# Performance work log

Measured on AMD Instinct MI355X. Metric: run time of the kernel, lower is better.

The kernel has to match this reference:

```python
import jax, jax.numpy as jnp
import numpy as np

K = 16       # patchsize
STRIDE = 4
C1 = 1e-6
C2 = 1e-6


def _unfold(x):
    # Mirrors nn.Unfold(kernel_size=16, stride=4) followed by
    # .view(a,b,k,k,-1).transpose(2,4): output (a,b,pt_num,k,k) where the
    # trailing (k,k) matrix is the TRANSPOSED patch (kw,kh), exactly as in torch.
    a, b, H, W = x.shape
    nh = (H - K) // STRIDE + 1
    nw = (W - K) // STRIDE + 1
    r = (jnp.arange(nh) * STRIDE)[:, None] + jnp.arange(K)[None, :]  # (nh,K)
    c = (jnp.arange(nw) * STRIDE)[:, None] + jnp.arange(K)[None, :]  # (nw,K)
    p = x[:, :, r[:, None, :, None], c[None, :, None, :]]  # (a,b,nh,nw,K,K) = (kh,kw)
    p = p.reshape(a, b, nh * nw, K, K)
    return jnp.swapaxes(p, -1, -2)  # transposed patch, matching transpose(2,4)


def _layer(ref_f, dist_f):
    # ref_f, dist_f: (a,b,H,W) feature maps of one VGG layer
    pr = _unfold(ref_f)   # (a,b,pt,K,K)
    pd = _unfold(dist_f)
    u_r, s_r, _ = jnp.linalg.svd(pr, full_matrices=False)  # u:(a,b,pt,K,K) s:(a,b,pt,K)
    u_d, s_d, _ = jnp.linalg.svd(pd, full_matrices=False)
    diff_s = (s_r - s_d) ** 2                               # (a,b,pt,K)
    # abs of elementwise U product summed over singular-vector index (sign-invariant)
    u_rd = jnp.abs(u_r * u_d).sum(-1)                       # (a,b,pt,K)
    wt = jnp.std(u_rd, axis=-1, ddof=1) / (jnp.mean(u_rd, axis=-1) + 1e-9)  # (a,b,pt)
    ds = (diff_s.sum(-1) * wt).mean(-1).mean(-1)            # (a,)
    # global luminance-similarity weighting
    xm = dist_f.mean(axis=(2, 3))                           # (a,b)
    ym = ref_f.mean(axis=(2, 3))
    s1 = (2.0 * xm * ym + C1) / (xm ** 2 + ym ** 2 + C2)
    glb = jnp.exp(-2.0 * s1.mean(axis=1))                   # (a,)
    return ds * glb


def setup_inputs() -> dict:
    key = jax.random.key(0)
    k1, k2, k3, k4 = jax.random.split(key, 4)
    return {
        "ref_feat3": jax.random.normal(k1, (4, 256, 64, 64), jnp.float32),
        "dist_feat3": jax.random.normal(k2, (4, 256, 64, 64), jnp.float32),
        "ref_feat4": jax.random.normal(k3, (4, 512, 32, 32), jnp.float32),
        "dist_feat4": jax.random.normal(k4, (4, 512, 32, 32), jnp.float32),
    }


def reference(ref_feat3, dist_feat3, ref_feat4, dist_feat4):
    # DMM accumulates the weighted singular-value distance over the two feature levels
    return _layer(ref_feat3, dist_feat3) + _layer(ref_feat4, dist_feat4)
```

## Files before the change

kernel.cpp:

```cpp
#include <hip/hip_runtime.h>
#include <math.h>

#define NSWEEPS 4

typedef _Float16 f16x2 __attribute__((ext_vector_type(2)));
typedef float    f32x2 __attribute__((ext_vector_type(2)));

__device__ __forceinline__ int h2i(f16x2 v) { int r; __builtin_memcpy(&r, &v, 4); return r; }
__device__ __forceinline__ f16x2 i2h(int v) { f16x2 r; __builtin_memcpy(&r, &v, 4); return r; }

__device__ __forceinline__ f32x2 rcp2(f32x2 v) {
  return f32x2{__builtin_amdgcn_rcpf(v.x), __builtin_amdgcn_rcpf(v.y)};
}
__device__ __forceinline__ f32x2 sqrt2(f32x2 v) {
  return f32x2{__builtin_amdgcn_sqrtf(v.x), __builtin_amdgcn_sqrtf(v.y)};
}
__device__ __forceinline__ f32x2 cpsgn2(f32x2 m, f32x2 s) {
  return f32x2{copysignf(m.x, s.x), copysignf(m.y, s.y)};
}

__device__ __forceinline__ float fshfl_xor(float v, int m) {
  return __shfl_xor(v, m, 64);
}

template<int R>
__device__ __forceinline__ int xexch_i(int iv) {
  if constexpr (R == 1)      return __builtin_amdgcn_update_dpp(iv, iv, 0x0B1, 0xF, 0xF, true);
  else if constexpr (R == 2) return __builtin_amdgcn_update_dpp(iv, iv, 0x04E, 0xF, 0xF, true);
  else if constexpr (R == 3) return __builtin_amdgcn_update_dpp(iv, iv, 0x01B, 0xF, 0xF, true);
  else if constexpr (R == 7) return __builtin_amdgcn_update_dpp(iv, iv, 0x141, 0xF, 0xF, true);
  else if constexpr (R == 8) return __builtin_amdgcn_update_dpp(iv, iv, 0x128, 0xF, 0xF, true);
  else                       return __builtin_amdgcn_ds_swizzle(iv, (R << 10) | 0x1F);
}
template<int R>
__device__ __forceinline__ float xexch(float v) {
  return __int_as_float(xexch_i<R>(__float_as_int(v)));
}

template<int R>
__device__ __forceinline__ void jround2p(f16x2 (&wa)[8], f16x2 (&wb)[8],
                                         f32x2 &nn, f32x2 &d, f32x2 &id) {
  const f32x2 on = {xexch<R>(nn.x), xexch<R>(nn.y)};
  const f32x2 od = {xexch<R>(d.x),  xexch<R>(d.y)};
  f16x2 oa[8], ob[8];
#pragma unroll
  for (int i = 0; i < 8; ++i) oa[i] = i2h(xexch_i<R>(h2i(wa[i])));
#pragma unroll
  for (int i = 0; i < 8; ++i) ob[i] = i2h(xexch_i<R>(h2i(wb[i])));

  float pa0 = 0.f, pa1 = 0.f, pa2 = 0.f, pa3 = 0.f;
  float pb0 = 0.f, pb1 = 0.f, pb2 = 0.f, pb3 = 0.f;
  pa0 = __builtin_amdgcn_fdot2(wa[0], oa[0], pa0, false);
  pa1 = __builtin_amdgcn_fdot2(wa[1], oa[1], pa1, false);
  pa2 = __builtin_amdgcn_fdot2(wa[2], oa[2], pa2, false);
  pa3 = __builtin_amdgcn_fdot2(wa[3], oa[3], pa3, false);
  pb0 = __builtin_amdgcn_fdot2(wb[0], ob[0], pb0, false);
  pb1 = __builtin_amdgcn_fdot2(wb[1], ob[1], pb1, false);
  pb2 = __builtin_amdgcn_fdot2(wb[2], ob[2], pb2, false);
  pb3 = __builtin_amdgcn_fdot2(wb[3], ob[3], pb3, false);
  pa0 = __builtin_amdgcn_fdot2(wa[4], oa[4], pa0, false);
  pa1 = __builtin_amdgcn_fdot2(wa[5], oa[5], pa1, false);
  pa2 = __builtin_amdgcn_fdot2(wa[6], oa[6], pa2, false);
  pa3 = __builtin_amdgcn_fdot2(wa[7], oa[7], pa3, false);
  pb0 = __builtin_amdgcn_fdot2(wb[4], ob[4], pb0, false);
  pb1 = __builtin_amdgcn_fdot2(wb[5], ob[5], pb1, false);
  pb2 = __builtin_amdgcn_fdot2(wb[6], ob[6], pb2, false);
  pb3 = __builtin_amdgcn_fdot2(wb[7], ob[7], pb3, false);
  const f32x2 dot = {(pa0 + pa1) + (pa2 + pa3), (pb0 + pb1) + (pb2 + pb3)};

  const f32x2 dod = d * od;
  const f32x2 apq = dot * dod;
  const f32x2 dl  = on - nn;
  const f32x2 p2  = apq + apq;
  const f32x2 rt  = sqrt2(dl * dl + p2 * p2 + 1e-37f);
  const f32x2 den = dl + cpsgn2(rt, dl);
  const f32x2 t   = p2 * rcp2(den);
  const f32x2 sec = sqrt2(t * t + 1.0f);
  const f32x2 c   = rcp2(sec);
  const f32x2 rc  = -t * (id * od);

  const _Float16 hra = (_Float16)rc.x;
  const _Float16 hrb = (_Float16)rc.y;
  const f16x2 ra = {hra, hra};
  const f16x2 rb = {hrb, hrb};
#pragma unroll
  for (int i = 0; i < 8; ++i) wa[i] = __builtin_elementwise_fma(ra, oa[i], wa[i]);
#pragma unroll
  for (int i = 0; i < 8; ++i) wb[i] = __builtin_elementwise_fma(rb, ob[i], wb[i]);
  d  *= c;
  id *= sec;
  nn  = nn - t * apq;
}

__device__ __forceinline__ void jsweep2p(f16x2 (&a)[8], f16x2 (&b)[8],
                                         f32x2 &nn, f32x2 &d, f32x2 &id) {
  jround2p<1>(a, b, nn, d, id);
  jround2p<2>(a, b, nn, d, id);
  jround2p<3>(a, b, nn, d, id);
  jround2p<4>(a, b, nn, d, id);
  jround2p<5>(a, b, nn, d, id);
  jround2p<6>(a, b, nn, d, id);
  jround2p<7>(a, b, nn, d, id);
  jround2p<8>(a, b, nn, d, id);
  jround2p<9>(a, b, nn, d, id);
  jround2p<10>(a, b, nn, d, id);
  jround2p<11>(a, b, nn, d, id);
  jround2p<12>(a, b, nn, d, id);
  jround2p<13>(a, b, nn, d, id);
  jround2p<14>(a, b, nn, d, id);
  jround2p<15>(a, b, nn, d, id);
  const _Float16 hda = (_Float16)d.x;
  const _Float16 hdb = (_Float16)d.y;
  const f16x2 sa = {hda, hda};
  const f16x2 sb = {hdb, hdb};
#pragma unroll
  for (int i = 0; i < 8; ++i) a[i] *= sa;
#pragma unroll
  for (int i = 0; i < 8; ++i) b[i] *= sb;
  d = f32x2{1.f, 1.f}; id = f32x2{1.f, 1.f};
}

__device__ __forceinline__ void load16(const float* __restrict__ src, float (&a)[16]) {
  const float4* p = (const float4*)src;
  float4 v0 = p[0], v1 = p[1], v2 = p[2], v3 = p[3];
  a[0] = v0.x; a[1] = v0.y; a[2]  = v0.z; a[3]  = v0.w;
  a[4] = v1.x; a[5] = v1.y; a[6]  = v1.z; a[7]  = v1.w;
  a[8] = v2.x; a[9] = v2.y; a[10] = v2.z; a[11] = v2.w;
  a[12] = v3.x; a[13] = v3.y; a[14] = v3.z; a[15] = v3.w;
}

__device__ __forceinline__ float sort16(float (&w)[16], const int lane, const int wl) {
  float s0 = 0.f, s1 = 0.f, s2v = 0.f, s3 = 0.f;
#pragma unroll
  for (int i = 0; i < 16; i += 4) {
    s0  = fmaf(w[i + 0], w[i + 0], s0);
    s1  = fmaf(w[i + 1], w[i + 1], s1);
    s2v = fmaf(w[i + 2], w[i + 2], s2v);
    s3  = fmaf(w[i + 3], w[i + 3], s3);
  }
  float s2 = (s0 + s1) + (s2v + s3);

  int rank = 0;
#pragma unroll
  for (int k = 0; k < 16; ++k) {
    const float vk = __shfl(s2, k, 16);
    rank += (vk > s2 || (vk == s2 && k < lane)) ? 1 : 0;
  }
  const int dst = (((wl & 48) | rank) << 2);
#pragma unroll
  for (int i = 0; i < 16; ++i)
    w[i] = __int_as_float(__builtin_amdgcn_ds_permute(dst, __float_as_int(w[i])));
  s2 = __int_as_float(__builtin_amdgcn_ds_permute(dst, __float_as_int(s2)));
  return s2;
}

template<int CH, int H, int W, int NH, int NW>
__global__ __launch_bounds__(256)
void svd_layer_kernel(const float* __restrict__ ref, const float* __restrict__ dist,
                      float* __restrict__ dsSum) {
  constexpr int P = NH * NW;
  const int tid  = threadIdx.x;
  const int lane = tid & 15;
  const int wl   = tid & 63;
  const int pid  = blockIdx.x * 16 + (tid >> 4);
  const int ai   = pid / (CH * P);
  const int rem  = pid - ai * (CH * P);
  const int ch   = rem / P;
  const int pp   = rem - ch * P;
  const int ih   = pp / NW;
  const int iw   = pp - ih * NW;
  const size_t off = (size_t)(ai * CH + ch) * (H * W) + (size_t)(ih * 4 + lane) * W + iw * 4;

  float tr[16], td[16];
  load16(ref + off, tr);
  load16(dist + off, td);

  float nnr = 0.f, nnd = 0.f;
#pragma unroll
  for (int i = 0; i < 16; ++i) { nnr = fmaf(tr[i], tr[i], nnr); nnd = fmaf(td[i], td[i], nnd); }

  f16x2 wr[8], wd[8];
#pragma unroll
  for (int i = 0; i < 8; ++i) {
    wr[i] = f16x2{(_Float16)tr[2 * i], (_Float16)tr[2 * i + 1]};
    wd[i] = f16x2{(_Float16)td[2 * i], (_Float16)td[2 * i + 1]};
  }

  f32x2 nn = {nnr, nnd};
  f32x2 d  = {1.f, 1.f};
  f32x2 id = {1.f, 1.f};
  for (int sw = 0; sw < NSWEEPS; ++sw) jsweep2p(wr, wd, nn, d, id);

  float ar[16], ad[16];
#pragma unroll
  for (int i = 0; i < 8; ++i) {
    ar[2 * i] = (float)wr[i][0]; ar[2 * i + 1] = (float)wr[i][1];
    ad[2 * i] = (float)wd[i][0]; ad[2 * i + 1] = (float)wd[i][1];
  }

  const float s2r = sort16(ar, lane, wl);
  const float s2d = sort16(ad, lane, wl);

  const float sigr = __builtin_amdgcn_sqrtf(s2r);
  const float sigd = __builtin_amdgcn_sqrtf(s2d);
  const float ddv = sigr - sigd;
  float diffs = ddv * ddv;
#pragma unroll
  for (int st = 1; st < 16; st <<= 1) diffs += fshfl_xor(diffs, st);

  const float fac = __builtin_amdgcn_rsqf(s2r * s2d);
  float prd[16];
#pragma unroll
  for (int i = 0; i < 16; ++i) prd[i] = fabsf(ar[i] * ad[i]) * fac;
#pragma unroll
  for (int st = 1; st < 16; st <<= 1) {
#pragma unroll
    for (int i = 0; i < 16; ++i) prd[i] += fshfl_xor(prd[i], st);
  }
  float sum = 0.0f, sumsq = 0.0f;
#pragma unroll
  for (int i = 0; i < 16; ++i) { sum += prd[i]; sumsq = fmaf(prd[i], prd[i], sumsq); }
  const float mean = sum * 0.0625f;
  float var = (sumsq - 16.0f * mean * mean) * (1.0f / 15.0f);
  var = fmaxf(var, 0.0f);
  const float wt  = __builtin_amdgcn_sqrtf(var) * __builtin_amdgcn_rcpf(mean + 1e-9f);
  const float val = diffs * wt;

  __shared__ float blk;
  if (tid == 0) blk = 0.0f;
  __syncthreads();
  if (lane == 0) atomicAdd(&blk, val);
  __syncthreads();
  if (tid == 0) atomicAdd(&dsSum[ai], blk);
}

template<int CH, int HW>
__global__ __launch_bounds__(256)
void glb_kernel(const float* __restrict__ ref, const float* __restrict__ dist,
                float* __restrict__ s1Sum) {
  const int bid = blockIdx.x;
  const int ai  = bid / CH;
  const float4* pr = (const float4*)(ref + (size_t)bid * HW);
  const float4* pd = (const float4*)(dist + (size_t)bid * HW);
  float sr = 0.0f, sd = 0.0f;
  for (int i = threadIdx.x; i < HW / 4; i += 256) {
    const float4 r = pr[i], d = pd[i];
    sr += (r.x + r.y) + (r.z + r.w);
    sd += (d.x + d.y) + (d.z + d.w);
  }
#pragma unroll
  for (int st = 32; st >= 1; st >>= 1) { sr += __shfl_xor(sr, st, 64); sd += __shfl_xor(sd, st, 64); }
  __shared__ float bufR[4], bufD[4];
  const int w = threadIdx.x >> 6;
  if ((threadIdx.x & 63) == 0) { bufR[w] = sr; bufD[w] = sd; }
  __syncthreads();
  if (threadIdx.x == 0) {
    const float ym = (bufR[0] + bufR[1] + bufR[2] + bufR[3]) * (1.0f / HW);
    const float xm = (bufD[0] + bufD[1] + bufD[2] + bufD[3]) * (1.0f / HW);
    const float s1 = (2.0f * xm * ym + 1e-6f) / (xm * xm + ym * ym + 1e-6f);
    atomicAdd(&s1Sum[ai], s1);
  }
}

__global__ void final_kernel(const float* __restrict__ ws, float* __restrict__ out) {
  const int ai = threadIdx.x;
  if (ai < 4) {
    const float ds3 = ws[ai]      * (1.0f / (256.0f * 169.0f));
    const float ds4 = ws[4 + ai]  * (1.0f / (512.0f * 25.0f));
    const float g3  = expf(-2.0f * ws[8 + ai]  * (1.0f / 256.0f));
    const float g4  = expf(-2.0f * ws[12 + ai] * (1.0f / 512.0f));
    out[ai] = ds3 * g3 + ds4 * g4;
  }
}

extern "C" void kernel_launch(void* const* d_in, const int* in_sizes, int n_in,
                              void* d_out, int out_size, void* d_ws, size_t ws_size,
                              hipStream_t stream) {
  const float* ref3  = (const float*)d_in[0];
  const float* dist3 = (const float*)d_in[1];
  const float* ref4  = (const float*)d_in[2];
  const float* dist4 = (const float*)d_in[3];
  float* ws  = (float*)d_ws;
  float* out = (float*)d_out;

  hipMemsetAsync(ws, 0, 16 * sizeof(float), stream);

  svd_layer_kernel<256, 64, 64, 13, 13><<<173056 / 16, 256, 0, stream>>>(ref3, dist3, ws + 0);
  svd_layer_kernel<512, 32, 32, 5, 5><<<51200 / 16, 256, 0, stream>>>(ref4, dist4, ws + 4);

  glb_kernel<256, 4096><<<4 * 256, 256, 0, stream>>>(ref3, dist3, ws + 8);
  glb_kernel<512, 1024><<<4 * 512, 256, 0, stream>>>(ref4, dist4, ws + 12);

  final_kernel<<<1, 64, 0, stream>>>(ws, out);
}
```

Measured before the change: 680.1 us.

## Fuse all layer kernels into one launch and shrink the post-Jacobi epilogue to fp16

Merges the two SVD kernels, the two global-mean kernels and the final combine into one kernel that dispatches on block index. A last-block atomic counter computes the output, which removes four extra kernel launches. The last sweep's scale-and-reset is dropped and the singular-vector norms are taken with fdot2 directly on packed fp16. The epilogue now sorts and reduces half-precision pairs with DPP exchanges instead of fp32 arrays and shuffles. This cuts register pressure and cross-lane traffic, at the cost of fp16 accuracy in the weight statistics and of relying on the counter plus threadfence for correct ordering.

```diff
diff --git a/kernel.cpp b/kernel.cpp
--- a/kernel.cpp
+++ b/kernel.cpp
@@ -8,6 +8,7 @@
 
 __device__ __forceinline__ int h2i(f16x2 v) { int r; __builtin_memcpy(&r, &v, 4); return r; }
 __device__ __forceinline__ f16x2 i2h(int v) { f16x2 r; __builtin_memcpy(&r, &v, 4); return r; }
+__device__ __forceinline__ f16x2 dup_h(float x) { _Float16 h = (_Float16)x; return f16x2{h, h}; }
 
 __device__ __forceinline__ f32x2 rcp2(f32x2 v) {
   return f32x2{__builtin_amdgcn_rcpf(v.x), __builtin_amdgcn_rcpf(v.y)};
@@ -79,10 +80,8 @@
   const f32x2 c   = rcp2(sec);
   const f32x2 rc  = -t * (id * od);
 
-  const _Float16 hra = (_Float16)rc.x;
-  const _Float16 hrb = (_Float16)rc.y;
-  const f16x2 ra = {hra, hra};
-  const f16x2 rb = {hrb, hrb};
+  const f16x2 ra = dup_h(rc.x);
+  const f16x2 rb = dup_h(rc.y);
 #pragma unroll
   for (int i = 0; i < 8; ++i) wa[i] = __builtin_elementwise_fma(ra, oa[i], wa[i]);
 #pragma unroll
@@ -92,8 +91,8 @@
   nn  = nn - t * apq;
 }
 
-__device__ __forceinline__ void jsweep2p(f16x2 (&a)[8], f16x2 (&b)[8],
-                                         f32x2 &nn, f32x2 &d, f32x2 &id) {
+__device__ __forceinline__ void jrounds(f16x2 (&a)[8], f16x2 (&b)[8],
+                                        f32x2 &nn, f32x2 &d, f32x2 &id) {
   jround2p<1>(a, b, nn, d, id);
   jround2p<2>(a, b, nn, d, id);
   jround2p<3>(a, b, nn, d, id);
@@ -109,15 +108,6 @@
   jround2p<13>(a, b, nn, d, id);
   jround2p<14>(a, b, nn, d, id);
   jround2p<15>(a, b, nn, d, id);
-  const _Float16 hda = (_Float16)d.x;
-  const _Float16 hdb = (_Float16)d.y;
-  const f16x2 sa = {hda, hda};
-  const f16x2 sb = {hdb, hdb};
-#pragma unroll
-  for (int i = 0; i < 8; ++i) a[i] *= sa;
-#pragma unroll
-  for (int i = 0; i < 8; ++i) b[i] *= sb;
-  d = f32x2{1.f, 1.f}; id = f32x2{1.f, 1.f};
 }
 
 __device__ __forceinline__ void load16(const float* __restrict__ src, float (&a)[16]) {
@@ -129,17 +119,8 @@
   a[12] = v3.x; a[13] = v3.y; a[14] = v3.z; a[15] = v3.w;
 }
 
-__device__ __forceinline__ float sort16(float (&w)[16], const int lane, const int wl) {
-  float s0 = 0.f, s1 = 0.f, s2v = 0.f, s3 = 0.f;
-#pragma unroll
-  for (int i = 0; i < 16; i += 4) {
-    s0  = fmaf(w[i + 0], w[i + 0], s0);
-    s1  = fmaf(w[i + 1], w[i + 1], s1);
-    s2v = fmaf(w[i + 2], w[i + 2], s2v);
-    s3  = fmaf(w[i + 3], w[i + 3], s3);
-  }
-  float s2 = (s0 + s1) + (s2v + s3);
-
+__device__ __forceinline__ float sort16p(f16x2 (&u)[8], float s2,
+                                         const int lane, const int wl) {
   int rank = 0;
 #pragma unroll
   for (int k = 0; k < 16; ++k) {
@@ -148,21 +129,20 @@
   }
   const int dst = (((wl & 48) | rank) << 2);
 #pragma unroll
-  for (int i = 0; i < 16; ++i)
-    w[i] = __int_as_float(__builtin_amdgcn_ds_permute(dst, __float_as_int(w[i])));
-  s2 = __int_as_float(__builtin_amdgcn_ds_permute(dst, __float_as_int(s2)));
-  return s2;
+  for (int i = 0; i < 8; ++i)
+    u[i] = i2h(__builtin_amdgcn_ds_permute(dst, h2i(u[i])));
+  return __int_as_float(__builtin_amdgcn_ds_permute(dst, __float_as_int(s2)));
 }
 
 template<int CH, int H, int W, int NH, int NW>
-__global__ __launch_bounds__(256)
-void svd_layer_kernel(const float* __restrict__ ref, const float* __restrict__ dist,
-                      float* __restrict__ dsSum) {
+__device__ __forceinline__ void svd_body(const float* __restrict__ ref,
+                                         const float* __restrict__ dist,
+                                         float* __restrict__ dsSum, int blk0) {
   constexpr int P = NH * NW;
   const int tid  = threadIdx.x;
   const int lane = tid & 15;
   const int wl   = tid & 63;
-  const int pid  = blockIdx.x * 16 + (tid >> 4);
+  const int pid  = (blockIdx.x - blk0) * 16 + (tid >> 4);
   const int ai   = pid / (CH * P);
   const int rem  = pid - ai * (CH * P);
   const int ch   = rem / P;
@@ -189,37 +169,66 @@
   f32x2 nn = {nnr, nnd};
   f32x2 d  = {1.f, 1.f};
   f32x2 id = {1.f, 1.f};
-  for (int sw = 0; sw < NSWEEPS; ++sw) jsweep2p(wr, wd, nn, d, id);
-
-  float ar[16], ad[16];
-#pragma unroll
-  for (int i = 0; i < 8; ++i) {
-    ar[2 * i] = (float)wr[i][0]; ar[2 * i + 1] = (float)wr[i][1];
-    ad[2 * i] = (float)wd[i][0]; ad[2 * i + 1] = (float)wd[i][1];
-  }
-
-  const float s2r = sort16(ar, lane, wl);
-  const float s2d = sort16(ad, lane, wl);
+#pragma unroll
+  for (int sw = 0; sw < NSWEEPS; ++sw) {
+    jrounds(wr, wd, nn, d, id);
+    if (sw < NSWEEPS - 1) {
+      const f16x2 sa = dup_h(d.x), sb = dup_h(d.y);
+#pragma unroll
+      for (int i = 0; i < 8; ++i) { wr[i] *= sa; wd[i] *= sb; }
+      d = f32x2{1.f, 1.f}; id = f32x2{1.f, 1.f};
+    }
+  }
+
+  float r0 = 0.f, r1 = 0.f, q0 = 0.f, q1 = 0.f;
+#pragma unroll
+  for (int i = 0; i < 8; i += 2) {
+    r0 = __builtin_amdgcn_fdot2(wr[i],     wr[i],     r0, false);
+    r1 = __builtin_amdgcn_fdot2(wr[i + 1], wr[i + 1], r1, false);
+    q0 = __builtin_amdgcn_fdot2(wd[i],     wd[i],     q0, false);
+    q1 = __builtin_amdgcn_fdot2(wd[i + 1], wd[i + 1], q1, false);
+  }
+  const float sw2r = r0 + r1, sw2d = q0 + q1;
+  float s2r = sw2r * (d.x * d.x);
+  float s2d = sw2d * (d.y * d.y);
+  const f16x2 ur_s = dup_h(__builtin_amdgcn_rsqf(sw2r + 1e-30f));
+  const f16x2 ud_s = dup_h(__builtin_amdgcn_rsqf(sw2d + 1e-30f));
+#pragma unroll
+  for (int i = 0; i < 8; ++i) { wr[i] *= ur_s; wd[i] *= ud_s; }
+
+  s2r = sort16p(wr, s2r, lane, wl);
+  s2d = sort16p(wd, s2d, lane, wl);
 
   const float sigr = __builtin_amdgcn_sqrtf(s2r);
   const float sigd = __builtin_amdgcn_sqrtf(s2d);
   const float ddv = sigr - sigd;
   float diffs = ddv * ddv;
-#pragma unroll
-  for (int st = 1; st < 16; st <<= 1) diffs += fshfl_xor(diffs, st);
-
-  const float fac = __builtin_amdgcn_rsqf(s2r * s2d);
-  float prd[16];
-#pragma unroll
-  for (int i = 0; i < 16; ++i) prd[i] = fabsf(ar[i] * ad[i]) * fac;
-#pragma unroll
-  for (int st = 1; st < 16; st <<= 1) {
-#pragma unroll
-    for (int i = 0; i < 16; ++i) prd[i] += fshfl_xor(prd[i], st);
-  }
-  float sum = 0.0f, sumsq = 0.0f;
-#pragma unroll
-  for (int i = 0; i < 16; ++i) { sum += prd[i]; sumsq = fmaf(prd[i], prd[i], sumsq); }
+  diffs += fshfl_xor(diffs, 1);
+  diffs += fshfl_xor(diffs, 2);
+  diffs += fshfl_xor(diffs, 4);
+  diffs += fshfl_xor(diffs, 8);
+
+  f16x2 prd[8];
+#pragma unroll
+  for (int i = 0; i < 8; ++i) prd[i] = i2h(h2i(wr[i] * wd[i]) & 0x7FFF7FFF);
+#pragma unroll
+  for (int i = 0; i < 8; ++i) prd[i] += i2h(xexch_i<1>(h2i(prd[i])));
+#pragma unroll
+  for (int i = 0; i < 8; ++i) prd[i] += i2h(xexch_i<2>(h2i(prd[i])));
+#pragma unroll
+  for (int i = 0; i < 8; ++i) prd[i] += i2h(xexch_i<4>(h2i(prd[i])));
+#pragma unroll
+  for (int i = 0; i < 8; ++i) prd[i] += i2h(xexch_i<8>(h2i(prd[i])));
+  const f16x2 one2 = {(_Float16)1.f, (_Float16)1.f};
+  float sA0 = 0.f, sA1 = 0.f, sQ0 = 0.f, sQ1 = 0.f;
+#pragma unroll
+  for (int i = 0; i < 8; i += 2) {
+    sA0 = __builtin_amdgcn_fdot2(prd[i],     one2,       sA0, false);
+    sA1 = __builtin_amdgcn_fdot2(prd[i + 1], one2,       sA1, false);
+    sQ0 = __builtin_amdgcn_fdot2(prd[i],     prd[i],     sQ0, false);
+    sQ1 = __builtin_amdgcn_fdot2(prd[i + 1], prd[i + 1], sQ1, false);
+  }
+  const float sum = sA0 + sA1, sumsq = sQ0 + sQ1;
   const float mean = sum * 0.0625f;
   float var = (sumsq - 16.0f * mean * mean) * (1.0f / 15.0f);
   var = fmaxf(var, 0.0f);
@@ -235,10 +244,10 @@
 }
 
 template<int CH, int HW>
-__global__ __launch_bounds__(256)
-void glb_kernel(const float* __restrict__ ref, const float* __restrict__ dist,
-                float* __restrict__ s1Sum) {
-  const int bid = blockIdx.x;
+__device__ __forceinline__ void glb_body(const float* __restrict__ ref,
+                                         const float* __restrict__ dist,
+                                         float* __restrict__ s1Sum, int blk0) {
+  const int bid = blockIdx.x - blk0;
   const int ai  = bid / CH;
   const float4* pr = (const float4*)(ref + (size_t)bid * HW);
   const float4* pd = (const float4*)(dist + (size_t)bid * HW);
@@ -262,14 +271,40 @@
   }
 }
 
-__global__ void final_kernel(const float* __restrict__ ws, float* __restrict__ out) {
-  const int ai = threadIdx.x;
-  if (ai < 4) {
-    const float ds3 = ws[ai]      * (1.0f / (256.0f * 169.0f));
-    const float ds4 = ws[4 + ai]  * (1.0f / (512.0f * 25.0f));
-    const float g3  = expf(-2.0f * ws[8 + ai]  * (1.0f / 256.0f));
-    const float g4  = expf(-2.0f * ws[12 + ai] * (1.0f / 512.0f));
-    out[ai] = ds3 * g3 + ds4 * g4;
+#define B3  10816
+#define G3B 1024
+#define B4  3200
+#define G4B 2048
+#define TOTB (B3 + G3B + B4 + G4B)
+
+__global__ __launch_bounds__(256)
+void mega_kernel(const float* __restrict__ ref3, const float* __restrict__ dist3,
+                 const float* __restrict__ ref4, const float* __restrict__ dist4,
+                 float* __restrict__ ws, float* __restrict__ out) {
+  const int b = blockIdx.x;
+  if (b < B3) {
+    svd_body<256, 64, 64, 13, 13>(ref3, dist3, ws + 0, 0);
+  } else if (b < B3 + G3B) {
+    glb_body<256, 4096>(ref3, dist3, ws + 8, B3);
+  } else if (b < B3 + G3B + B4) {
+    svd_body<512, 32, 32, 5, 5>(ref4, dist4, ws + 4, B3 + G3B);
+  } else {
+    glb_body<512, 1024>(ref4, dist4, ws + 12, B3 + G3B + B4);
+  }
+
+  __threadfence();
+  if (threadIdx.x == 0) {
+    const unsigned t = atomicAdd((unsigned*)(ws + 16), 1u);
+    if (t == TOTB - 1) {
+#pragma unroll
+      for (int ai = 0; ai < 4; ++ai) {
+        const float ds3 = atomicAdd(&ws[ai],      0.f) * (1.0f / (256.0f * 169.0f));
+        const float ds4 = atomicAdd(&ws[4 + ai],  0.f) * (1.0f / (512.0f * 25.0f));
+        const float g3  = expf(-2.0f * atomicAdd(&ws[8 + ai],  0.f) * (1.0f / 256.0f));
+        const float g4  = expf(-2.0f * atomicAdd(&ws[12 + ai], 0.f) * (1.0f / 512.0f));
+        out[ai] = ds3 * g3 + ds4 * g4;
+      }
+    }
   }
 }
 
@@ -283,13 +318,6 @@
   float* ws  = (float*)d_ws;
   float* out = (float*)d_out;
 
-  hipMemsetAsync(ws, 0, 16 * sizeof(float), stream);
-
-  svd_layer_kernel<256, 64, 64, 13, 13><<<173056 / 16, 256, 0, stream>>>(ref3, dist3, ws + 0);
-  svd_layer_kernel<512, 32, 32, 5, 5><<<51200 / 16, 256, 0, stream>>>(ref4, dist4, ws + 4);
-
-  glb_kernel<256, 4096><<<4 * 256, 256, 0, stream>>>(ref3, dist3, ws + 8);
-  glb_kernel<512, 1024><<<4 * 512, 256, 0, stream>>>(ref4, dist4, ws + 12);
-
-  final_kernel<<<1, 64, 0, stream>>>(ws, out);
-}
+  hipMemsetAsync(ws, 0, 128, stream);
+  mega_kernel<<<TOTB, 256, 0, stream>>>(ref3, dist3, ref4, dist4, ws, out);
+}
```

New measurement: 1.795 ms. 164% more time.
